# Optimization experiments

Hardware: AMD Instinct MI355X
Metric: run time of the kernel (lower is better)

## Reference

```python
import jax, jax.numpy as jnp
import numpy as np

DIM = 512
NUM_HEADS = 4
SCALE = 1.0 / np.sqrt(DIM)  # note: module scales by 1/sqrt(dim), not 1/sqrt(head_dim)


def setup_inputs() -> dict:
    key = jax.random.key(0)
    k1, k2, k3, k4, k5, k6 = jax.random.split(key, 6)
    B, N, M, C = 8, 2048, 2048, DIM
    bound = 1.0 / np.sqrt(C)
    return {
        "F1": jax.random.normal(k1, (B, N, C), dtype=jnp.float32),
        "F2": jax.random.normal(k2, (B, M, C), dtype=jnp.float32),
        "W_qkv": jax.random.uniform(k3, (C, C), jnp.float32, -bound, bound),
        "b_qkv": jax.random.uniform(k4, (C,), jnp.float32, -bound, bound),
        "W_proj": jax.random.uniform(k5, (C, C), jnp.float32, -bound, bound),
        "b_proj": jax.random.uniform(k6, (C,), jnp.float32, -bound, bound),
    }


def reference(F1, F2, W_qkv, b_qkv, W_proj, b_proj):
    B, N, C = F1.shape
    M = F2.shape[1]
    H, D = NUM_HEADS, C // NUM_HEADS
    # shared qkv projection (same weights for q, k and v in the original module)
    q = (F1 @ W_qkv + b_qkv).reshape(B, N, H, D)  # queries from F1
    kv = (F2 @ W_qkv + b_qkv).reshape(B, M, H, D)  # keys == values from F2
    attn = jnp.einsum("bnhd,bmhd->bhnm", q * SCALE, kv)
    attn = jax.nn.softmax(attn, axis=-1)
    x = jnp.einsum("bhnm,bmhd->bnhd", attn, kv).reshape(B, N, C)
    return x @ W_proj + b_proj
```

## Files before the change

### kernel.cpp

```cpp
#include <hip/hip_runtime.h>
#include <math.h>


typedef __attribute__((ext_vector_type(8))) short s16x8;
typedef __attribute__((ext_vector_type(4))) float f32x4;

#define C_DIM 512
#define HDIM  128
#define NROWS 16384
#define SCALE_Q 0.04419417382415922f
#define LOG2E   1.4426950408889634f

__device__ __forceinline__ unsigned short f2bf(float f) {
    union { float f; unsigned u; } v; v.f = f;
    unsigned r = v.u + 0x7fffu + ((v.u >> 16) & 1u);
    return (unsigned short)(r >> 16);
}

__device__ __forceinline__ void async16(const void* g, void* l) {
    __builtin_amdgcn_global_load_lds(
        (const __attribute__((address_space(1))) void*)g,
        (__attribute__((address_space(3))) void*)l, 16, 0, 0);
}

__global__ __launch_bounds__(256)
void conv_bf16_2(const float* __restrict__ s0, const float* __restrict__ s1,
                 unsigned short* __restrict__ d0, unsigned short* __restrict__ d1,
                 int n8) {
    const float* src = blockIdx.y ? s1 : s0;
    unsigned short* dst = blockIdx.y ? d1 : d0;
    int i = blockIdx.x * 256 + threadIdx.x;
    if (i >= n8) return;
    float4 a = ((const float4*)src)[2 * i];
    float4 b = ((const float4*)src)[2 * i + 1];
    union { unsigned short us[8]; uint4 v; } o;
    o.us[0] = f2bf(a.x); o.us[1] = f2bf(a.y); o.us[2] = f2bf(a.z); o.us[3] = f2bf(a.w);
    o.us[4] = f2bf(b.x); o.us[5] = f2bf(b.y); o.us[6] = f2bf(b.z); o.us[7] = f2bf(b.w);
    ((uint4*)dst)[i] = o.v;
}

__global__ __launch_bounds__(256)
void wconv_t2(const float* __restrict__ W0, const float* __restrict__ W1,
              unsigned short* __restrict__ T0, unsigned short* __restrict__ T1) {
    const float* W = blockIdx.z ? W1 : W0;
    unsigned short* Wt = blockIdx.z ? T1 : T0;
    __shared__ float t[64][65];
    const int k0 = blockIdx.y * 64, n0 = blockIdx.x * 64;
    const int c = threadIdx.x & 63, r0 = threadIdx.x >> 6;
#pragma unroll
    for (int r = r0; r < 64; r += 4)
        t[r][c] = W[(size_t)(k0 + r) * C_DIM + n0 + c];
    __syncthreads();
#pragma unroll
    for (int r = r0; r < 64; r += 4)
        Wt[(size_t)(n0 + r) * C_DIM + k0 + c] = f2bf(t[c][r]);
}

__global__ __launch_bounds__(256)
void kv_transpose(const unsigned short* __restrict__ KV,
                  unsigned short* __restrict__ KVT) {
    __shared__ unsigned short t[64][66];
    const int key0 = blockIdx.x * 64;
    const int d0   = blockIdx.y * 64;
    const int bh   = blockIdx.z;
    const int b    = bh >> 2, h = bh & 3;
    const int c = threadIdx.x & 63, r0 = threadIdx.x >> 6;
    const unsigned short* src = KV + ((size_t)(b * 2048 + key0)) * C_DIM + h * HDIM + d0;
#pragma unroll
    for (int r = r0; r < 64; r += 4)
        t[r][c] = src[(size_t)r * C_DIM + c];
    __syncthreads();
    unsigned short* dst = KVT + ((size_t)(bh * HDIM + d0)) * 2048 + key0;
#pragma unroll
    for (int r = r0; r < 64; r += 4)
        dst[(size_t)r * 2048 + c] = t[c][r];
}

template <int OUT_BF16>
__global__ __launch_bounds__(256, 3)
void gemm_bt(const unsigned short* __restrict__ A,
             const unsigned short* __restrict__ Bt,
             const float* __restrict__ bias,
             void* __restrict__ Cv, float oscTop, int topRows) {
    __shared__ __align__(16) unsigned short As[128][64];
    __shared__ __align__(16) unsigned short Bs[128][64];

    const int tid  = threadIdx.x;
    const int wid  = tid >> 6;
    const int lane = tid & 63;
    const int lr   = lane & 15;
    const int quad = lane >> 4;
    const int wm   = wid >> 1;
    const int wn   = wid & 1;
    const int rowBase = blockIdx.y * 128;
    const int colBase = blockIdx.x * 128;
    const int srow = lane >> 3;
    const int soff = srow * C_DIM + (((lane & 7) ^ (srow & 7)) * 8);
    const float osc = (rowBase < topRows) ? oscTop : 1.0f;

    f32x4 acc[4][4];
#pragma unroll
    for (int i = 0; i < 4; i++)
#pragma unroll
        for (int j = 0; j < 4; j++) acc[i][j] = (f32x4)0.0f;

    for (int kt = 0; kt < 8; kt++) {
        const int k0 = kt * 64;
        __syncthreads();
#pragma unroll
        for (int i = 0; i < 4; i++) {
            const int R = wid * 32 + i * 8;
            async16(A  + (size_t)(rowBase + R) * C_DIM + k0 + soff, &As[R][0]);
            async16(Bt + (size_t)(colBase + R) * C_DIM + k0 + soff, &Bs[R][0]);
        }
        __syncthreads();

#pragma unroll
        for (int s = 0; s < 2; s++) {
            s16x8 af[4], bf[4];
#pragma unroll
            for (int i = 0; i < 4; i++)
                af[i] = *(const s16x8*)&As[wm * 64 + i * 16 + lr][((s * 4 + quad) ^ (lr & 7)) * 8];
#pragma unroll
            for (int j = 0; j < 4; j++)
                bf[j] = *(const s16x8*)&Bs[wn * 64 + j * 16 + lr][((s * 4 + quad) ^ (lr & 7)) * 8];
#pragma unroll
            for (int i = 0; i < 4; i++)
#pragma unroll
                for (int j = 0; j < 4; j++)
                    acc[i][j] = __builtin_amdgcn_mfma_f32_16x16x32_bf16(af[i], bf[j], acc[i][j], 0, 0, 0);
        }
    }

    float bcol[4];
#pragma unroll
    for (int j = 0; j < 4; j++)
        bcol[j] = bias[colBase + wn * 64 + j * 16 + lr];
#pragma unroll
    for (int i = 0; i < 4; i++) {
#pragma unroll
        for (int j = 0; j < 4; j++) {
            const int col = colBase + wn * 64 + j * 16 + lr;
#pragma unroll
            for (int r = 0; r < 4; r++) {
                const int row = rowBase + wm * 64 + i * 16 + quad * 4 + r;
                float v = (acc[i][j][r] + bcol[j]) * osc;
                if (OUT_BF16)
                    ((unsigned short*)Cv)[(size_t)row * C_DIM + col] = f2bf(v);
                else
                    ((float*)Cv)[(size_t)row * C_DIM + col] = v;
            }
        }
    }
}

__global__ __launch_bounds__(256, 2)
void cross_attn(const unsigned short* __restrict__ Q,
                const unsigned short* __restrict__ KV,
                const unsigned short* __restrict__ KVT,
                unsigned short* __restrict__ X) {
    __shared__ __align__(16) unsigned short Kt[2][64][128];
    __shared__ __align__(16) unsigned short Vt[2][128][64];

    const int tid  = threadIdx.x;
    const int wid  = tid >> 6;
    const int lane = tid & 63;
    const int lr   = lane & 15;
    const int quad = lane >> 4;

    const int wg   = blockIdx.x;
    const int xcd  = wg & 7;
    const int slot = wg >> 3;
    const int p    = xcd + 8 * (slot & 3);
    const int xblk = slot >> 2;
    const int b    = p >> 2;
    const int h    = p & 3;
    const int hoff = h * HDIM;
    const size_t qrow0  = (size_t)b * 2048 + xblk * 128 + wid * 32;
    const size_t kvrow0 = (size_t)b * 2048;

    s16x8 qf[2][4];
#pragma unroll
    for (int i = 0; i < 2; i++)
#pragma unroll
        for (int kk = 0; kk < 4; kk++)
            qf[i][kk] = *(const s16x8*)(Q + (qrow0 + i * 16 + lr) * C_DIM + hoff + kk * 32 + quad * 8);

    const unsigned short* pK[4];
    const unsigned short* pV[4];
#pragma unroll
    for (int a = 0; a < 4; a++) {
        const int R   = wid * 16 + a * 4 + (lane >> 4);
        const int key = 32 * (R >> 5) + 8 * ((R >> 2) & 3) + 4 * ((R >> 4) & 1) + (R & 3);
        const int pp  = lane & 15;
        const int ck  = (pp & 8) | ((pp ^ (R & 7)) & 7);
        pK[a] = KV + (kvrow0 + key) * C_DIM + hoff + ck * 8;
        const int d  = wid * 32 + a * 8 + (lane >> 3);
        const int cv = (lane & 7) ^ (lane >> 3);
        pV[a] = KVT + ((size_t)((b * 4 + h) * HDIM + d)) * 2048 + cv * 8;
    }

    f32x4 O[2][8];
#pragma unroll
    for (int i = 0; i < 2; i++)
#pragma unroll
        for (int dt = 0; dt < 8; dt++) O[i][dt] = (f32x4)0.0f;
    float lacc[2];
    lacc[0] = 0.0f; lacc[1] = 0.0f;

#pragma unroll
    for (int a = 0; a < 4; a++) {
        async16(pK[a], &Kt[0][wid * 16 + a * 4][0]);
        async16(pV[a], &Vt[0][wid * 32 + a * 8][0]);
    }

    for (int kt = 0; kt < 32; kt++) {
        const int cur = kt & 1;
        if (kt < 31) {
            const size_t key0 = (size_t)(kt + 1) * 64;
#pragma unroll
            for (int a = 0; a < 4; a++) {
                async16(pK[a] + key0 * C_DIM, &Kt[cur ^ 1][wid * 16 + a * 4][0]);
                async16(pV[a] + key0,         &Vt[cur ^ 1][wid * 32 + a * 8][0]);
            }
            asm volatile("s_waitcnt vmcnt(8)" ::: "memory");
        } else {
            asm volatile("s_waitcnt vmcnt(0)" ::: "memory");
        }
        __builtin_amdgcn_sched_barrier(0);
        __builtin_amdgcn_s_barrier();
        __builtin_amdgcn_sched_barrier(0);

        f32x4 s[2][4];
#pragma unroll
        for (int i = 0; i < 2; i++)
#pragma unroll
            for (int j = 0; j < 4; j++) s[i][j] = (f32x4)0.0f;
#pragma unroll
        for (int kk = 0; kk < 4; kk++) {
#pragma unroll
            for (int j = 0; j < 4; j++) {
                s16x8 kf = *(const s16x8*)&Kt[cur][j * 16 + lr][((kk * 4 + quad) ^ (lr & 7)) * 8];
                s[0][j] = __builtin_amdgcn_mfma_f32_16x16x32_bf16(kf, qf[0][kk], s[0][j], 0, 0, 0);
                s[1][j] = __builtin_amdgcn_mfma_f32_16x16x32_bf16(kf, qf[1][kk], s[1][j], 0, 0, 0);
            }
        }

        s16x8 pa[2][2];
#pragma unroll
        for (int i = 0; i < 2; i++) {
#pragma unroll
            for (int kk = 0; kk < 2; kk++) {
                float p0 = __builtin_amdgcn_exp2f(s[i][2 * kk][0]);
                float p1 = __builtin_amdgcn_exp2f(s[i][2 * kk][1]);
                float p2 = __builtin_amdgcn_exp2f(s[i][2 * kk][2]);
                float p3 = __builtin_amdgcn_exp2f(s[i][2 * kk][3]);
                float p4 = __builtin_amdgcn_exp2f(s[i][2 * kk + 1][0]);
                float p5 = __builtin_amdgcn_exp2f(s[i][2 * kk + 1][1]);
                float p6 = __builtin_amdgcn_exp2f(s[i][2 * kk + 1][2]);
                float p7 = __builtin_amdgcn_exp2f(s[i][2 * kk + 1][3]);
                lacc[i] += ((p0 + p1) + (p2 + p3)) + ((p4 + p5) + (p6 + p7));
                union { unsigned short us[8]; s16x8 v; } pu;
                pu.us[0] = f2bf(p0); pu.us[1] = f2bf(p1);
                pu.us[2] = f2bf(p2); pu.us[3] = f2bf(p3);
                pu.us[4] = f2bf(p4); pu.us[5] = f2bf(p5);
                pu.us[6] = f2bf(p6); pu.us[7] = f2bf(p7);
                pa[i][kk] = pu.v;
            }
        }

#pragma unroll
        for (int kk = 0; kk < 2; kk++) {
#pragma unroll
            for (int dt = 0; dt < 8; dt++) {
                s16x8 vf = *(const s16x8*)&Vt[cur][dt * 16 + lr][((kk * 4 + quad) ^ (lr & 7)) * 8];
                O[0][dt] = __builtin_amdgcn_mfma_f32_16x16x32_bf16(pa[0][kk], vf, O[0][dt], 0, 0, 0);
                O[1][dt] = __builtin_amdgcn_mfma_f32_16x16x32_bf16(pa[1][kk], vf, O[1][dt], 0, 0, 0);
            }
        }

        asm volatile("s_waitcnt lgkmcnt(0)" ::: "memory");
        __builtin_amdgcn_sched_barrier(0);
        __builtin_amdgcn_s_barrier();
        __builtin_amdgcn_sched_barrier(0);
    }

#pragma unroll
    for (int i = 0; i < 2; i++) {
        float l = lacc[i];
        l += __shfl_xor(l, 16);
        l += __shfl_xor(l, 32);
#pragma unroll
        for (int r = 0; r < 4; r++) {
            const float inv = 1.0f / __shfl(l, quad * 4 + r);
            const size_t row = (qrow0 + i * 16 + quad * 4 + r) * C_DIM + hoff;
#pragma unroll
            for (int dt = 0; dt < 8; dt++)
                X[row + dt * 16 + lr] = f2bf(O[i][dt][r] * inv);
        }
    }
}

extern "C" void kernel_launch(void* const* d_in, const int* in_sizes, int n_in,
                              void* d_out, int out_size, void* d_ws, size_t ws_size,
                              hipStream_t stream) {
    const float* F1     = (const float*)d_in[0];
    const float* F2     = (const float*)d_in[1];
    const float* W_qkv  = (const float*)d_in[2];
    const float* b_qkv  = (const float*)d_in[3];
    const float* W_proj = (const float*)d_in[4];
    const float* b_proj = (const float*)d_in[5];
    float* out = (float*)d_out;

    const size_t NC = (size_t)NROWS * C_DIM;
    unsigned short* F1b = (unsigned short*)d_ws;
    unsigned short* F2b = F1b + NC;
    unsigned short* Qw  = F2b + NC;
    unsigned short* KVw = Qw  + NC;
    unsigned short* Wqt = KVw + NC;
    unsigned short* Wpt = Wqt + C_DIM * C_DIM;
    unsigned short* Xw  = F1b;
    unsigned short* KVT = F2b;

    dim3 blk(256);

    conv_bf16_2<<<dim3(NC / 8 / 256, 2), blk, 0, stream>>>(F1, F2, F1b, F2b, (int)(NC / 8));
    wconv_t2<<<dim3(8, 8, 2), blk, 0, stream>>>(W_qkv, W_proj, Wqt, Wpt);

    gemm_bt<1><<<dim3(4, 256), blk, 0, stream>>>(F1b, Wqt, b_qkv, Qw, SCALE_Q * LOG2E, NROWS);
    kv_transpose<<<dim3(32, 2, 32), blk, 0, stream>>>(KVw, KVT);
    cross_attn<<<dim3(512), blk, 0, stream>>>(Qw, KVw, KVT, Xw);
    gemm_bt<0><<<dim3(4, 128), blk, 0, stream>>>(Xw, Wpt, b_proj, out, 1.0f, 0);
}
```

Before: 240.2 us.

## Double per-wave query tile and deepen K/V prefetch to four LDS stages

Each wave now handles 64 query rows instead of 32, so every K/V fragment read from LDS feeds four MFMA row tiles, halving LDS traffic per query. The grid drops to 256 blocks with launch bounds of one block per CU. K/V staging goes from two to four LDS buffers with a prefetch distance of two, which lets the trailing per-iteration barrier be removed. The softmax/PV step is split into two key halves to limit live score registers. The cost is fewer resident waves per CU for hiding latency, plus higher register and LDS use.

```diff
diff --git a/kernel.cpp b/kernel.cpp
--- a/kernel.cpp
+++ b/kernel.cpp
@@ -154,13 +154,13 @@
     }
 }
 
-__global__ __launch_bounds__(256, 2)
+__global__ __launch_bounds__(256, 1)
 void cross_attn(const unsigned short* __restrict__ Q,
                 const unsigned short* __restrict__ KV,
                 const unsigned short* __restrict__ KVT,
                 unsigned short* __restrict__ X) {
-    __shared__ __align__(16) unsigned short Kt[2][64][128];
-    __shared__ __align__(16) unsigned short Vt[2][128][64];
+    __shared__ __align__(16) unsigned short Kt[4][64][128];
+    __shared__ __align__(16) unsigned short Vt[4][128][64];
 
     const int tid  = threadIdx.x;
     const int wid  = tid >> 6;
@@ -176,12 +176,12 @@
     const int b    = p >> 2;
     const int h    = p & 3;
     const int hoff = h * HDIM;
-    const size_t qrow0  = (size_t)b * 2048 + xblk * 128 + wid * 32;
+    const size_t qrow0  = (size_t)b * 2048 + xblk * 256 + wid * 64;
     const size_t kvrow0 = (size_t)b * 2048;
 
-    s16x8 qf[2][4];
-#pragma unroll
-    for (int i = 0; i < 2; i++)
+    s16x8 qf[4][4];
+#pragma unroll
+    for (int i = 0; i < 4; i++)
 #pragma unroll
         for (int kk = 0; kk < 4; kk++)
             qf[i][kk] = *(const s16x8*)(Q + (qrow0 + i * 16 + lr) * C_DIM + hoff + kk * 32 + quad * 8);
@@ -200,29 +200,37 @@
         pV[a] = KVT + ((size_t)((b * 4 + h) * HDIM + d)) * 2048 + cv * 8;
     }
 
-    f32x4 O[2][8];
-#pragma unroll
-    for (int i = 0; i < 2; i++)
+    f32x4 O[4][8];
+#pragma unroll
+    for (int i = 0; i < 4; i++)
 #pragma unroll
         for (int dt = 0; dt < 8; dt++) O[i][dt] = (f32x4)0.0f;
-    float lacc[2];
-    lacc[0] = 0.0f; lacc[1] = 0.0f;
-
-#pragma unroll
-    for (int a = 0; a < 4; a++) {
-        async16(pK[a], &Kt[0][wid * 16 + a * 4][0]);
-        async16(pV[a], &Vt[0][wid * 32 + a * 8][0]);
+    float lacc[4];
+#pragma unroll
+    for (int i = 0; i < 4; i++) lacc[i] = 0.0f;
+
+#pragma unroll
+    for (int t = 0; t < 2; t++) {
+        const size_t key0 = (size_t)t * 64;
+#pragma unroll
+        for (int a = 0; a < 4; a++) {
+            async16(pK[a] + key0 * C_DIM, &Kt[t][wid * 16 + a * 4][0]);
+            async16(pV[a] + key0,         &Vt[t][wid * 32 + a * 8][0]);
+        }
     }
 
     for (int kt = 0; kt < 32; kt++) {
-        const int cur = kt & 1;
-        if (kt < 31) {
-            const size_t key0 = (size_t)(kt + 1) * 64;
+        const int cur = kt & 3;
+        if (kt < 30) {
+            const int nbuf = (kt + 2) & 3;
+            const size_t key0 = (size_t)(kt + 2) * 64;
 #pragma unroll
             for (int a = 0; a < 4; a++) {
-                async16(pK[a] + key0 * C_DIM, &Kt[cur ^ 1][wid * 16 + a * 4][0]);
-                async16(pV[a] + key0,         &Vt[cur ^ 1][wid * 32 + a * 8][0]);
-            }
+                async16(pK[a] + key0 * C_DIM, &Kt[nbuf][wid * 16 + a * 4][0]);
+                async16(pV[a] + key0,         &Vt[nbuf][wid * 32 + a * 8][0]);
+            }
+            asm volatile("s_waitcnt vmcnt(16)" ::: "memory");
+        } else if (kt == 30) {
             asm volatile("s_waitcnt vmcnt(8)" ::: "memory");
         } else {
             asm volatile("s_waitcnt vmcnt(0)" ::: "memory");
@@ -231,62 +239,56 @@
         __builtin_amdgcn_s_barrier();
         __builtin_amdgcn_sched_barrier(0);
 
-        f32x4 s[2][4];
-#pragma unroll
-        for (int i = 0; i < 2; i++)
-#pragma unroll
-            for (int j = 0; j < 4; j++) s[i][j] = (f32x4)0.0f;
-#pragma unroll
-        for (int kk = 0; kk < 4; kk++) {
-#pragma unroll
-            for (int j = 0; j < 4; j++) {
-                s16x8 kf = *(const s16x8*)&Kt[cur][j * 16 + lr][((kk * 4 + quad) ^ (lr & 7)) * 8];
-                s[0][j] = __builtin_amdgcn_mfma_f32_16x16x32_bf16(kf, qf[0][kk], s[0][j], 0, 0, 0);
-                s[1][j] = __builtin_amdgcn_mfma_f32_16x16x32_bf16(kf, qf[1][kk], s[1][j], 0, 0, 0);
-            }
-        }
-
-        s16x8 pa[2][2];
-#pragma unroll
-        for (int i = 0; i < 2; i++) {
-#pragma unroll
-            for (int kk = 0; kk < 2; kk++) {
-                float p0 = __builtin_amdgcn_exp2f(s[i][2 * kk][0]);
-                float p1 = __builtin_amdgcn_exp2f(s[i][2 * kk][1]);
-                float p2 = __builtin_amdgcn_exp2f(s[i][2 * kk][2]);
-                float p3 = __builtin_amdgcn_exp2f(s[i][2 * kk][3]);
-                float p4 = __builtin_amdgcn_exp2f(s[i][2 * kk + 1][0]);
-                float p5 = __builtin_amdgcn_exp2f(s[i][2 * kk + 1][1]);
-                float p6 = __builtin_amdgcn_exp2f(s[i][2 * kk + 1][2]);
-                float p7 = __builtin_amdgcn_exp2f(s[i][2 * kk + 1][3]);
+#pragma unroll
+        for (int half = 0; half < 2; half++) {
+            f32x4 s[4][2];
+#pragma unroll
+            for (int i = 0; i < 4; i++) {
+                s[i][0] = (f32x4)0.0f; s[i][1] = (f32x4)0.0f;
+            }
+#pragma unroll
+            for (int kk = 0; kk < 4; kk++) {
+#pragma unroll
+                for (int jh = 0; jh < 2; jh++) {
+                    s16x8 kf = *(const s16x8*)&Kt[cur][(half * 2 + jh) * 16 + lr][((kk * 4 + quad) ^ (lr & 7)) * 8];
+#pragma unroll
+                    for (int i = 0; i < 4; i++)
+                        s[i][jh] = __builtin_amdgcn_mfma_f32_16x16x32_bf16(kf, qf[i][kk], s[i][jh], 0, 0, 0);
+                }
+            }
+
+            s16x8 pa[4];
+#pragma unroll
+            for (int i = 0; i < 4; i++) {
+                float p0 = __builtin_amdgcn_exp2f(s[i][0][0]);
+                float p1 = __builtin_amdgcn_exp2f(s[i][0][1]);
+                float p2 = __builtin_amdgcn_exp2f(s[i][0][2]);
+                float p3 = __builtin_amdgcn_exp2f(s[i][0][3]);
+                float p4 = __builtin_amdgcn_exp2f(s[i][1][0]);
+                float p5 = __builtin_amdgcn_exp2f(s[i][1][1]);
+                float p6 = __builtin_amdgcn_exp2f(s[i][1][2]);
+                float p7 = __builtin_amdgcn_exp2f(s[i][1][3]);
                 lacc[i] += ((p0 + p1) + (p2 + p3)) + ((p4 + p5) + (p6 + p7));
                 union { unsigned short us[8]; s16x8 v; } pu;
                 pu.us[0] = f2bf(p0); pu.us[1] = f2bf(p1);
                 pu.us[2] = f2bf(p2); pu.us[3] = f2bf(p3);
                 pu.us[4] = f2bf(p4); pu.us[5] = f2bf(p5);
                 pu.us[6] = f2bf(p6); pu.us[7] = f2bf(p7);
-                pa[i][kk] = pu.v;
-            }
-        }
-
-#pragma unroll
-        for (int kk = 0; kk < 2; kk++) {
+                pa[i] = pu.v;
+            }
+
 #pragma unroll
             for (int dt = 0; dt < 8; dt++) {
-                s16x8 vf = *(const s16x8*)&Vt[cur][dt * 16 + lr][((kk * 4 + quad) ^ (lr & 7)) * 8];
-                O[0][dt] = __builtin_amdgcn_mfma_f32_16x16x32_bf16(pa[0][kk], vf, O[0][dt], 0, 0, 0);
-                O[1][dt] = __builtin_amdgcn_mfma_f32_16x16x32_bf16(pa[1][kk], vf, O[1][dt], 0, 0, 0);
-            }
-        }
-
-        asm volatile("s_waitcnt lgkmcnt(0)" ::: "memory");
-        __builtin_amdgcn_sched_barrier(0);
-        __builtin_amdgcn_s_barrier();
-        __builtin_amdgcn_sched_barrier(0);
-    }
-
-#pragma unroll
-    for (int i = 0; i < 2; i++) {
+                s16x8 vf = *(const s16x8*)&Vt[cur][dt * 16 + lr][((half * 4 + quad) ^ (lr & 7)) * 8];
+#pragma unroll
+                for (int i = 0; i < 4; i++)
+                    O[i][dt] = __builtin_amdgcn_mfma_f32_16x16x32_bf16(pa[i], vf, O[i][dt], 0, 0, 0);
+            }
+        }
+    }
+
+#pragma unroll
+    for (int i = 0; i < 4; i++) {
         float l = lacc[i];
         l += __shfl_xor(l, 16);
         l += __shfl_xor(l, 32);
@@ -329,6 +331,6 @@
 
     gemm_bt<1><<<dim3(4, 256), blk, 0, stream>>>(F1b, Wqt, b_qkv, Qw, SCALE_Q * LOG2E, NROWS);
     kv_transpose<<<dim3(32, 2, 32), blk, 0, stream>>>(KVw, KVT);
-    cross_attn<<<dim3(512), blk, 0, stream>>>(Qw, KVw, KVT, Xw);
+    cross_attn<<<dim3(256), blk, 0, stream>>>(Qw, KVw, KVT, Xw);
     gemm_bt<0><<<dim3(4, 128), blk, 0, stream>>>(Xw, Wpt, b_proj, out, 1.0f, 0);
 }
```

Result: slower. 260.4 us (+8.4%).

## Widen attention blocks to 8 waves with a 4-buffer prefetch-2 K/V pipeline

Applied to the files above, without the earlier changes.

The attention kernel now runs 512-thread blocks covering 256 query rows, so each staged K/V tile is shared by twice as many waves and the grid shrinks to 256 blocks. K/V staging moves from a double buffer to a four-buffer ring with a prefetch distance of two. That allows one barrier per tile instead of two, and the explicit LDS wait is dropped. s_setprio is raised around the MFMA sections so matrix work is favoured over other waves. In exchange, LDS use rises to 128KB per block, which likely limits each CU to one block and halves resident waves, so overlap now depends more on the deeper pipeline than on occupancy.

```diff
diff --git a/kernel.cpp b/kernel.cpp
--- a/kernel.cpp
+++ b/kernel.cpp
@@ -154,13 +154,13 @@
     }
 }
 
-__global__ __launch_bounds__(256, 2)
+__global__ __launch_bounds__(512, 2)
 void cross_attn(const unsigned short* __restrict__ Q,
                 const unsigned short* __restrict__ KV,
                 const unsigned short* __restrict__ KVT,
                 unsigned short* __restrict__ X) {
-    __shared__ __align__(16) unsigned short Kt[2][64][128];
-    __shared__ __align__(16) unsigned short Vt[2][128][64];
+    __shared__ __align__(16) unsigned short Kt[4][64][128];
+    __shared__ __align__(16) unsigned short Vt[4][128][64];
 
     const int tid  = threadIdx.x;
     const int wid  = tid >> 6;
@@ -176,7 +176,7 @@
     const int b    = p >> 2;
     const int h    = p & 3;
     const int hoff = h * HDIM;
-    const size_t qrow0  = (size_t)b * 2048 + xblk * 128 + wid * 32;
+    const size_t qrow0  = (size_t)b * 2048 + xblk * 256 + wid * 32;
     const size_t kvrow0 = (size_t)b * 2048;
 
     s16x8 qf[2][4];
@@ -186,16 +186,16 @@
         for (int kk = 0; kk < 4; kk++)
             qf[i][kk] = *(const s16x8*)(Q + (qrow0 + i * 16 + lr) * C_DIM + hoff + kk * 32 + quad * 8);
 
-    const unsigned short* pK[4];
-    const unsigned short* pV[4];
-#pragma unroll
-    for (int a = 0; a < 4; a++) {
-        const int R   = wid * 16 + a * 4 + (lane >> 4);
+    const unsigned short* pK[2];
+    const unsigned short* pV[2];
+#pragma unroll
+    for (int a = 0; a < 2; a++) {
+        const int R   = wid * 8 + a * 4 + (lane >> 4);
         const int key = 32 * (R >> 5) + 8 * ((R >> 2) & 3) + 4 * ((R >> 4) & 1) + (R & 3);
         const int pp  = lane & 15;
         const int ck  = (pp & 8) | ((pp ^ (R & 7)) & 7);
         pK[a] = KV + (kvrow0 + key) * C_DIM + hoff + ck * 8;
-        const int d  = wid * 32 + a * 8 + (lane >> 3);
+        const int d  = wid * 16 + a * 8 + (lane >> 3);
         const int cv = (lane & 7) ^ (lane >> 3);
         pV[a] = KVT + ((size_t)((b * 4 + h) * HDIM + d)) * 2048 + cv * 8;
     }
@@ -208,34 +208,22 @@
     float lacc[2];
     lacc[0] = 0.0f; lacc[1] = 0.0f;
 
-#pragma unroll
-    for (int a = 0; a < 4; a++) {
-        async16(pK[a], &Kt[0][wid * 16 + a * 4][0]);
-        async16(pV[a], &Vt[0][wid * 32 + a * 8][0]);
-    }
-
-    for (int kt = 0; kt < 32; kt++) {
-        const int cur = kt & 1;
-        if (kt < 31) {
-            const size_t key0 = (size_t)(kt + 1) * 64;
-#pragma unroll
-            for (int a = 0; a < 4; a++) {
-                async16(pK[a] + key0 * C_DIM, &Kt[cur ^ 1][wid * 16 + a * 4][0]);
-                async16(pV[a] + key0,         &Vt[cur ^ 1][wid * 32 + a * 8][0]);
-            }
-            asm volatile("s_waitcnt vmcnt(8)" ::: "memory");
-        } else {
-            asm volatile("s_waitcnt vmcnt(0)" ::: "memory");
-        }
-        __builtin_amdgcn_sched_barrier(0);
-        __builtin_amdgcn_s_barrier();
-        __builtin_amdgcn_sched_barrier(0);
-
+    auto STAGE = [&](int t, int buf) {
+        const size_t key0 = (size_t)t * 64;
+#pragma unroll
+        for (int a = 0; a < 2; a++) {
+            async16(pK[a] + key0 * C_DIM, &Kt[buf][wid * 8 + a * 4][0]);
+            async16(pV[a] + key0,         &Vt[buf][wid * 16 + a * 8][0]);
+        }
+    };
+
+    auto COMPUTE = [&](int cur) {
         f32x4 s[2][4];
 #pragma unroll
         for (int i = 0; i < 2; i++)
 #pragma unroll
             for (int j = 0; j < 4; j++) s[i][j] = (f32x4)0.0f;
+        __builtin_amdgcn_s_setprio(1);
 #pragma unroll
         for (int kk = 0; kk < 4; kk++) {
 #pragma unroll
@@ -245,6 +233,7 @@
                 s[1][j] = __builtin_amdgcn_mfma_f32_16x16x32_bf16(kf, qf[1][kk], s[1][j], 0, 0, 0);
             }
         }
+        __builtin_amdgcn_s_setprio(0);
 
         s16x8 pa[2][2];
 #pragma unroll
@@ -269,6 +258,7 @@
             }
         }
 
+        __builtin_amdgcn_s_setprio(1);
 #pragma unroll
         for (int kk = 0; kk < 2; kk++) {
 #pragma unroll
@@ -278,12 +268,46 @@
                 O[1][dt] = __builtin_amdgcn_mfma_f32_16x16x32_bf16(pa[1][kk], vf, O[1][dt], 0, 0, 0);
             }
         }
-
-        asm volatile("s_waitcnt lgkmcnt(0)" ::: "memory");
+        __builtin_amdgcn_s_setprio(0);
+    };
+
+    STAGE(0, 0);
+    STAGE(1, 1);
+
+#pragma unroll 4
+    for (int kt = 0; kt < 28; kt++) {
+        STAGE(kt + 2, (kt + 2) & 3);
+        asm volatile("s_waitcnt vmcnt(8)" ::: "memory");
         __builtin_amdgcn_sched_barrier(0);
         __builtin_amdgcn_s_barrier();
         __builtin_amdgcn_sched_barrier(0);
-    }
+        COMPUTE(kt & 3);
+    }
+    STAGE(30, 2);
+    asm volatile("s_waitcnt vmcnt(8)" ::: "memory");
+    __builtin_amdgcn_sched_barrier(0);
+    __builtin_amdgcn_s_barrier();
+    __builtin_amdgcn_sched_barrier(0);
+    COMPUTE(0);
+
+    STAGE(31, 3);
+    asm volatile("s_waitcnt vmcnt(8)" ::: "memory");
+    __builtin_amdgcn_sched_barrier(0);
+    __builtin_amdgcn_s_barrier();
+    __builtin_amdgcn_sched_barrier(0);
+    COMPUTE(1);
+
+    asm volatile("s_waitcnt vmcnt(4)" ::: "memory");
+    __builtin_amdgcn_sched_barrier(0);
+    __builtin_amdgcn_s_barrier();
+    __builtin_amdgcn_sched_barrier(0);
+    COMPUTE(2);
+
+    asm volatile("s_waitcnt vmcnt(0)" ::: "memory");
+    __builtin_amdgcn_sched_barrier(0);
+    __builtin_amdgcn_s_barrier();
+    __builtin_amdgcn_sched_barrier(0);
+    COMPUTE(3);
 
 #pragma unroll
     for (int i = 0; i < 2; i++) {
@@ -329,6 +353,6 @@
 
     gemm_bt<1><<<dim3(4, 256), blk, 0, stream>>>(F1b, Wqt, b_qkv, Qw, SCALE_Q * LOG2E, NROWS);
     kv_transpose<<<dim3(32, 2, 32), blk, 0, stream>>>(KVw, KVT);
-    cross_attn<<<dim3(512), blk, 0, stream>>>(Qw, KVw, KVT, Xw);
+    cross_attn<<<dim3(256), dim3(512), 0, stream>>>(Qw, KVw, KVT, Xw);
     gemm_bt<0><<<dim3(4, 128), blk, 0, stream>>>(Xw, Wpt, b_proj, out, 1.0f, 0);
 }
```

After: 239.3 us. Within noise of the previous version (-0.4%).
